# Kernel optimization log

Hardware: AMD Instinct MI355X
Metric: run time of the kernel (lower is better)

Reference implementation:

```python
import jax, jax.numpy as jnp
import numpy as np

B, S, D, H, OPS = 1024, 512, 128, 128, 16
V2 = 64000  # vocabulary_size * 2


def _lstm_last(emb, lengths, W_ih, W_hh, b_ih, b_hh, h0, c0):
    # emb: [B, S, D]; returns hidden state at step lengths-1 for each sample: [B, H]
    bsz = emb.shape[0]
    x = jnp.swapaxes(emb, 0, 1)  # [S, B, D]
    h = jnp.broadcast_to(h0[0], (bsz, h0.shape[-1]))  # learnable init state, expanded over batch
    c = jnp.broadcast_to(c0[0], (bsz, c0.shape[-1]))

    def step(carry, x_t):
        h, c = carry
        gates = x_t @ W_ih.T + b_ih + h @ W_hh.T + b_hh  # [B, 4H]
        i, f, g, o = jnp.split(gates, 4, axis=-1)  # torch LSTM gate order: i, f, g, o
        i = jax.nn.sigmoid(i); f = jax.nn.sigmoid(f)
        g = jnp.tanh(g); o = jax.nn.sigmoid(o)
        c = f * c + i * g
        h = o * jnp.tanh(c)
        return (h, c), h

    _, hs = jax.lax.scan(step, (h, c), x)  # hs: [S, B, H]
    t = jnp.maximum(lengths, 1) - 1  # last valid step per ragged sequence
    return hs[t, jnp.arange(bsz)]  # [B, H]


def setup_inputs() -> dict:
    key = jax.random.key(0)
    ks = jax.random.split(key, 12)
    sc = 0.05
    return {
        "tokens": jax.random.randint(ks[0], (B, S), 0, V2, dtype=jnp.int32),
        "lengths": jax.random.randint(ks[1], (B,), 1, S + 1, dtype=jnp.int32),
        "operator_onehot": jax.random.uniform(ks[2], (B, OPS), dtype=jnp.float32),
        "embedding": jax.random.normal(ks[3], (V2, D), dtype=jnp.float32) * sc,
        "W_ih": jax.random.normal(ks[4], (4 * H, D), dtype=jnp.float32) * sc,
        "W_hh": jax.random.normal(ks[5], (4 * H, H), dtype=jnp.float32) * sc,
        "b_ih": jax.random.normal(ks[6], (4 * H,), dtype=jnp.float32) * sc,
        "b_hh": jax.random.normal(ks[7], (4 * H,), dtype=jnp.float32) * sc,
        "h0": jnp.zeros((1, 1, H), dtype=jnp.float32),
        "c0": jnp.zeros((1, 1, H), dtype=jnp.float32),
        "lin_W": jax.random.normal(ks[8], (2, H + OPS), dtype=jnp.float32) * sc,
        "lin_b": jax.random.normal(ks[9], (2,), dtype=jnp.float32) * sc,
    }


def reference(tokens, lengths, operator_onehot, embedding, W_ih, W_hh, b_ih, b_hh, h0, c0, lin_W, lin_b):
    emb = jax.nn.relu(embedding[tokens])  # [B, S, D] embedding lookup + ReLU
    h_last = jax.nn.relu(_lstm_last(emb, lengths, W_ih, W_hh, b_ih, b_hh, h0, c0))  # [B, H]
    combined = jnp.concatenate([h_last, operator_onehot], axis=1)  # feature union
    return combined @ lin_W.T + lin_b  # [B, 2] logits (training mode: no sigmoid)
```

## Files before the change

kernel.cpp:

```cpp
#include <hip/hip_runtime.h>
#include <hip/hip_bf16.h>

#define NB    1024
#define SEQ   512
#define DIM   128
#define HID   128
#define NOPS  16
#define FEAT  144
#define BQ    4
#define AST   144
#define XST   578

typedef __bf16 bf16x8 __attribute__((ext_vector_type(8)));
typedef float  floatx4 __attribute__((ext_vector_type(4)));

__device__ __forceinline__ float gate_s(float aL, float aH, float ka) {
    const float kS = -1.4426950408889634f;
    const float arg = __builtin_fmaf(kS, aL, __builtin_fmaf(kS, aH, ka));
    return __builtin_amdgcn_rcpf(1.0f + __builtin_amdgcn_exp2f(arg));
}
__device__ __forceinline__ float gate_t(float aL, float aH, float ka) {
    const float kT = -2.8853900817779268f;
    const float arg = __builtin_fmaf(kT, aL, __builtin_fmaf(kT, aH, ka));
    return 2.0f * __builtin_amdgcn_rcpf(1.0f + __builtin_amdgcn_exp2f(arg)) - 1.0f;
}
__device__ __forceinline__ float tanh_c(float x) {
    const float kT = -2.8853900817779268f;
    return 2.0f * __builtin_amdgcn_rcpf(1.0f + __builtin_amdgcn_exp2f(kT * x)) - 1.0f;
}

__device__ __forceinline__ void block_sync_lds() {
    asm volatile("s_waitcnt lgkmcnt(0)\n\ts_barrier" ::: "memory");
}

__global__ __launch_bounds__(512, 2)
void lstm_fused(const int* __restrict__ tokens, const int* __restrict__ lengths,
                const float* __restrict__ onehot, const float* __restrict__ emb,
                const float* __restrict__ Wih, const float* __restrict__ Whh,
                const float* __restrict__ bih, const float* __restrict__ bhh,
                const float* __restrict__ h0, const float* __restrict__ c0,
                const float* __restrict__ linW, const float* __restrict__ linb,
                float* __restrict__ out)
{
    __shared__ __align__(16) __bf16 xbuf[8 * XST];
    __shared__ __align__(16) __bf16 hbuf[2 * BQ * AST];
    __shared__ __align__(16) float  hlbuf[BQ * HID];
    __shared__ __align__(16) int    tkbuf[BQ * SEQ];

    const int tid  = threadIdx.x;
    const int wave = tid >> 6;
    const int lane = tid & 63;
    const int quad = lane >> 4;
    const int lrow = lane & 15;
    const int bid  = blockIdx.x;

    bf16x8 wfx[4][4], wfh[4][4];
#pragma unroll
    for (int gt = 0; gt < 4; ++gt) {
        const int g = gt * 128 + wave * 16 + lrow;
#pragma unroll
        for (int kt = 0; kt < 4; ++kt) {
            const float* sx = Wih + g * DIM + kt * 32 + quad * 8;
            const float* sh = Whh + g * HID + kt * 32 + quad * 8;
            float4 a = *(const float4*)(sx);
            float4 b = *(const float4*)(sx + 4);
            bf16x8 v;
            v[0] = (__bf16)a.x; v[1] = (__bf16)a.y; v[2] = (__bf16)a.z; v[3] = (__bf16)a.w;
            v[4] = (__bf16)b.x; v[5] = (__bf16)b.y; v[6] = (__bf16)b.z; v[7] = (__bf16)b.w;
            wfx[gt][kt] = v;
            a = *(const float4*)(sh);
            b = *(const float4*)(sh + 4);
            v[0] = (__bf16)a.x; v[1] = (__bf16)a.y; v[2] = (__bf16)a.z; v[3] = (__bf16)a.w;
            v[4] = (__bf16)b.x; v[5] = (__bf16)b.y; v[6] = (__bf16)b.z; v[7] = (__bf16)b.w;
            wfh[gt][kt] = v;
        }
    }

    const int uu = wave * 16 + lrow;
    const int bq = bid * BQ + quad;
    int lenq = lengths[bq]; if (lenq < 1) lenq = 1;
    const int tlast = lenq - 1;

    int Lmax = 0;
#pragma unroll
    for (int s2 = 0; s2 < BQ; ++s2) {
        int l2 = lengths[bid * BQ + s2]; if (l2 < 1) l2 = 1;
        Lmax = (l2 > Lmax) ? l2 : Lmax;
    }

    const float kS = -1.4426950408889634f;
    const float kT = -2.8853900817779268f;
    const float karg0 = kS * (bih[0 * 128 + uu] + bhh[0 * 128 + uu]);
    const float karg1 = kS * (bih[1 * 128 + uu] + bhh[1 * 128 + uu]);
    const float karg2 = kT * (bih[2 * 128 + uu] + bhh[2 * 128 + uu]);
    const float karg3 = kS * (bih[3 * 128 + uu] + bhh[3 * 128 + uu]);

    float c  = c0[uu];
    float hl = 0.0f;

    const int m  = tid >> 7;
    const int u  = tid & 127;
    const int bm = bid * BQ + m;
    const int sm = m * AST + u;

    {
        const int4 tv = *(const int4*)(tokens + (size_t)bid * (BQ * SEQ) + tid * 4);
        *(int4*)(&tkbuf[tid * 4]) = tv;
    }

    hbuf[sm] = (__bf16)h0[u];
    const int* tokm = tokens + (size_t)bm * SEQ;
#pragma unroll
    for (int k = 0; k < 8; ++k) {
        float ek = emb[(size_t)tokm[k] * DIM + u];
        xbuf[k * XST + sm] = (__bf16)fmaxf(ek, 0.0f);
    }
    float e0 = emb[(size_t)tokm[8]  * DIM + u];
    float e1 = emb[(size_t)tokm[9]  * DIM + u];
    float e2 = emb[(size_t)tokm[10] * DIM + u];
    float e3 = emb[(size_t)tokm[11] * DIM + u];
    int   tk = tokm[12];

#define EREG(OFF) ((OFF) == 0 ? e0 : (OFF) == 1 ? e1 : (OFF) == 2 ? e2 : e3)

    const int xfbase = (lrow & 3) * XST + (lrow >> 2) * AST + quad * 8;
    const __bf16* const xfp[2] = { &xbuf[xfbase], &xbuf[4 * XST + xfbase] };
    const int habase = (lrow >> 2) * AST + quad * 8;
    const __bf16* const hf[2] = { &hbuf[habase], &hbuf[BQ * AST + habase] };
    __bf16* const hw[2] = { &hbuf[quad * AST + uu], &hbuf[BQ * AST + quad * AST + uu] };
    __bf16* const xw = &xbuf[sm];

    __syncthreads();

    const floatx4 zc = {0.0f, 0.0f, 0.0f, 0.0f};

    floatx4 xga[4], xgb[4];
#define XBLOCK(GRP, XGN) do {                                                        \
        bf16x8 af_[4];                                                               \
        _Pragma("unroll") for (int kt = 0; kt < 4; ++kt)                             \
            af_[kt] = *(const bf16x8*)(xfp[GRP] + kt * 32);                          \
        _Pragma("unroll") for (int gt = 0; gt < 4; ++gt)                             \
            XGN[gt] = __builtin_amdgcn_mfma_f32_16x16x32_bf16(af_[0], wfx[gt][0], zc, 0, 0, 0); \
        _Pragma("unroll") for (int kt = 1; kt < 4; ++kt)                             \
            _Pragma("unroll") for (int gt = 0; gt < 4; ++gt)                         \
                XGN[gt] = __builtin_amdgcn_mfma_f32_16x16x32_bf16(af_[kt], wfx[gt][kt], XGN[gt], 0, 0, 0); \
    } while (0)

    XBLOCK(0, xga);
    block_sync_lds();

#define STEP(G, OFF, XGC, XGN) do {                                                  \
        const int t  = ts + OFF;                                                     \
        bf16x8 ah_[4];                                                               \
        _Pragma("unroll") for (int kt = 0; kt < 4; ++kt)                             \
            ah_[kt] = *(const bf16x8*)(hf[OFF & 1] + kt * 32);                       \
        if (t + 8 < SEQ)         \
            xw[(4 * (G) + (OFF)) * XST] = (__bf16)fmaxf(EREG(OFF), 0.0f);            \
        if (t + 12 < SEQ)                                    \
            EREG(OFF) = emb[(size_t)tk * DIM + u];                                   \
        tk = tkbuf[m * SEQ + (((t + 13) < SEQ) ? (t + 13) : (SEQ - 1))];             \
        floatx4 aL[4], aH[4];                                                        \
        _Pragma("unroll") for (int gt = 0; gt < 4; ++gt)                             \
            aL[gt] = __builtin_amdgcn_mfma_f32_16x16x32_bf16(ah_[0], wfh[gt][0], XGC[gt], 0, 0, 0); \
        _Pragma("unroll") for (int gt = 0; gt < 4; ++gt)                             \
            aH[gt] = __builtin_amdgcn_mfma_f32_16x16x32_bf16(ah_[2], wfh[gt][2], zc, 0, 0, 0); \
        _Pragma("unroll") for (int gt = 0; gt < 4; ++gt)                             \
            aL[gt] = __builtin_amdgcn_mfma_f32_16x16x32_bf16(ah_[1], wfh[gt][1], aL[gt], 0, 0, 0); \
        _Pragma("unroll") for (int gt = 0; gt < 4; ++gt)                             \
            aH[gt] = __builtin_amdgcn_mfma_f32_16x16x32_bf16(ah_[3], wfh[gt][3], aH[gt], 0, 0, 0); \
        if (OFF == 0) { XBLOCK(1 - (G), XGN); }                                      \
        const float ii = gate_s(aL[0][OFF], aH[0][OFF], karg0);                      \
        const float ff = gate_s(aL[1][OFF], aH[1][OFF], karg1);                      \
        const float g2 = gate_t(aL[2][OFF], aH[2][OFF], karg2);                      \
        const float oo = gate_s(aL[3][OFF], aH[3][OFF], karg3);                      \
        c = ff * c + ii * g2;                                                        \
        const float h = oo * tanh_c(c);                                              \
        if (t == tlast) hl = fmaxf(h, 0.0f);                                         \
        *hw[1 - (OFF & 1)] = (__bf16)h;                                              \
        block_sync_lds();                                                            \
    } while (0)

    for (int ts8 = 0; ts8 < Lmax; ts8 += 8) {
        {
            const int ts = ts8;
            STEP(0, 0, xga, xgb); STEP(0, 1, xga, xgb);
            STEP(0, 2, xga, xgb); STEP(0, 3, xga, xgb);
        }
        {
            const int ts = ts8 + 4;
            STEP(1, 0, xgb, xga); STEP(1, 1, xgb, xga);
            STEP(1, 2, xgb, xga); STEP(1, 3, xgb, xga);
        }
    }
#undef STEP
#undef XBLOCK
#undef EREG

    hlbuf[quad * HID + uu] = hl;
    __syncthreads();
    if (tid < 2 * BQ) {
        const int mm = tid >> 1, kk = tid & 1;
        const int bb = bid * BQ + mm;
        float a2 = linb[kk];
        for (int q = 0; q < HID; ++q)
            a2 += hlbuf[mm * HID + q] * linW[kk * FEAT + q];
        for (int o = 0; o < NOPS; ++o)
            a2 += onehot[bb * NOPS + o] * linW[kk * FEAT + HID + o];
        out[bb * 2 + kk] = a2;
    }
}

extern "C" void kernel_launch(void* const* d_in, const int* in_sizes, int n_in,
                              void* d_out, int out_size, void* d_ws, size_t ws_size,
                              hipStream_t stream) {
    const int*   tokens  = (const int*)d_in[0];
    const int*   lengths = (const int*)d_in[1];
    const float* onehot  = (const float*)d_in[2];
    const float* emb     = (const float*)d_in[3];
    const float* Wih     = (const float*)d_in[4];
    const float* Whh     = (const float*)d_in[5];
    const float* bih     = (const float*)d_in[6];
    const float* bhh     = (const float*)d_in[7];
    const float* h0      = (const float*)d_in[8];
    const float* c0      = (const float*)d_in[9];
    const float* linW    = (const float*)d_in[10];
    const float* linb    = (const float*)d_in[11];
    float* out = (float*)d_out;
    (void)in_sizes; (void)n_in; (void)out_size; (void)d_ws; (void)ws_size;

    lstm_fused<<<dim3(NB / BQ), dim3(512), 0, stream>>>(
        tokens, lengths, onehot, emb, Wih, Whh, bih, bhh, h0, c0, linW, linb, out);
}
```

Measured before the change: 435.3 us.

## Spread next-group input projection MFMAs across the four recurrent steps

The input-projection block for the next group of four timesteps, previously issued all at once (16 MFMAs) in the first step, is now split so each step issues four MFMAs for one K slice. This balances MFMA work across steps on the serial recurrence critical path. The token buffer is also padded with zeros per row so the clamped index computation for the lookahead token fetch can be dropped. Correctness relies on each K slice of the x buffer being final before its step reads it, which the existing per-step barriers should ensure.

```diff
diff --git a/kernel.cpp b/kernel.cpp
--- a/kernel.cpp
+++ b/kernel.cpp
@@ -10,6 +10,7 @@
 #define BQ    4
 #define AST   144
 #define XST   578
+#define TKST  (SEQ + 16)
 
 typedef __bf16 bf16x8 __attribute__((ext_vector_type(8)));
 typedef float  floatx4 __attribute__((ext_vector_type(4)));
@@ -45,7 +46,7 @@
     __shared__ __align__(16) __bf16 xbuf[8 * XST];
     __shared__ __align__(16) __bf16 hbuf[2 * BQ * AST];
     __shared__ __align__(16) float  hlbuf[BQ * HID];
-    __shared__ __align__(16) int    tkbuf[BQ * SEQ];
+    __shared__ __align__(16) int    tkbuf[BQ * TKST];
 
     const int tid  = threadIdx.x;
     const int wave = tid >> 6;
@@ -104,8 +105,10 @@
     const int sm = m * AST + u;
 
     {
-        const int4 tv = *(const int4*)(tokens + (size_t)bid * (BQ * SEQ) + tid * 4);
-        *(int4*)(&tkbuf[tid * 4]) = tv;
+        const int4 tv = *(const int4*)(tokens + (size_t)bm * SEQ + (tid & 127) * 4);
+        *(int4*)(&tkbuf[m * TKST + (tid & 127) * 4]) = tv;
+        if (tid < BQ * 16)
+            tkbuf[(tid >> 4) * TKST + SEQ + (tid & 15)] = 0;
     }
 
     hbuf[sm] = (__bf16)h0[u];
@@ -135,40 +138,50 @@
     const floatx4 zc = {0.0f, 0.0f, 0.0f, 0.0f};
 
     floatx4 xga[4], xgb[4];
-#define XBLOCK(GRP, XGN) do {                                                        \
-        bf16x8 af_[4];                                                               \
-        _Pragma("unroll") for (int kt = 0; kt < 4; ++kt)                             \
-            af_[kt] = *(const bf16x8*)(xfp[GRP] + kt * 32);                          \
-        _Pragma("unroll") for (int gt = 0; gt < 4; ++gt)                             \
-            XGN[gt] = __builtin_amdgcn_mfma_f32_16x16x32_bf16(af_[0], wfx[gt][0], zc, 0, 0, 0); \
-        _Pragma("unroll") for (int kt = 1; kt < 4; ++kt)                             \
-            _Pragma("unroll") for (int gt = 0; gt < 4; ++gt)                         \
-                XGN[gt] = __builtin_amdgcn_mfma_f32_16x16x32_bf16(af_[kt], wfx[gt][kt], XGN[gt], 0, 0, 0); \
-    } while (0)
-
-    XBLOCK(0, xga);
+    {
+        bf16x8 af_[4];
+#pragma unroll
+        for (int kt = 0; kt < 4; ++kt)
+            af_[kt] = *(const bf16x8*)(xfp[0] + kt * 32);
+#pragma unroll
+        for (int gt = 0; gt < 4; ++gt)
+            xga[gt] = __builtin_amdgcn_mfma_f32_16x16x32_bf16(af_[0], wfx[gt][0], zc, 0, 0, 0);
+#pragma unroll
+        for (int kt = 1; kt < 4; ++kt)
+#pragma unroll
+            for (int gt = 0; gt < 4; ++gt)
+                xga[gt] = __builtin_amdgcn_mfma_f32_16x16x32_bf16(af_[kt], wfx[gt][kt], xga[gt], 0, 0, 0);
+    }
     block_sync_lds();
 
 #define STEP(G, OFF, XGC, XGN) do {                                                  \
         const int t  = ts + OFF;                                                     \
-        bf16x8 ah_[4];                                                               \
-        _Pragma("unroll") for (int kt = 0; kt < 4; ++kt)                             \
-            ah_[kt] = *(const bf16x8*)(hf[OFF & 1] + kt * 32);                       \
+        bf16x8 ah0 = *(const bf16x8*)(hf[OFF & 1] + 0 * 32);                         \
+        bf16x8 ah2 = *(const bf16x8*)(hf[OFF & 1] + 2 * 32);                         \
+        bf16x8 ah1 = *(const bf16x8*)(hf[OFF & 1] + 1 * 32);                         \
+        bf16x8 ah3 = *(const bf16x8*)(hf[OFF & 1] + 3 * 32);                         \
+        bf16x8 ax_ = *(const bf16x8*)(xfp[1 - (G)] + (OFF) * 32);                    \
         if (t + 8 < SEQ)         \
             xw[(4 * (G) + (OFF)) * XST] = (__bf16)fmaxf(EREG(OFF), 0.0f);            \
         if (t + 12 < SEQ)                                    \
             EREG(OFF) = emb[(size_t)tk * DIM + u];                                   \
-        tk = tkbuf[m * SEQ + (((t + 13) < SEQ) ? (t + 13) : (SEQ - 1))];             \
+        tk = tkbuf[m * TKST + t + 13];                                               \
         floatx4 aL[4], aH[4];                                                        \
         _Pragma("unroll") for (int gt = 0; gt < 4; ++gt)                             \
-            aL[gt] = __builtin_amdgcn_mfma_f32_16x16x32_bf16(ah_[0], wfh[gt][0], XGC[gt], 0, 0, 0); \
-        _Pragma("unroll") for (int gt = 0; gt < 4; ++gt)                             \
-            aH[gt] = __builtin_amdgcn_mfma_f32_16x16x32_bf16(ah_[2], wfh[gt][2], zc, 0, 0, 0); \
-        _Pragma("unroll") for (int gt = 0; gt < 4; ++gt)                             \
-            aL[gt] = __builtin_amdgcn_mfma_f32_16x16x32_bf16(ah_[1], wfh[gt][1], aL[gt], 0, 0, 0); \
-        _Pragma("unroll") for (int gt = 0; gt < 4; ++gt)                             \
-            aH[gt] = __builtin_amdgcn_mfma_f32_16x16x32_bf16(ah_[3], wfh[gt][3], aH[gt], 0, 0, 0); \
-        if (OFF == 0) { XBLOCK(1 - (G), XGN); }                                      \
+            aL[gt] = __builtin_amdgcn_mfma_f32_16x16x32_bf16(ah0, wfh[gt][0], XGC[gt], 0, 0, 0); \
+        _Pragma("unroll") for (int gt = 0; gt < 4; ++gt)                             \
+            aH[gt] = __builtin_amdgcn_mfma_f32_16x16x32_bf16(ah2, wfh[gt][2], zc, 0, 0, 0); \
+        _Pragma("unroll") for (int gt = 0; gt < 4; ++gt)                             \
+            aL[gt] = __builtin_amdgcn_mfma_f32_16x16x32_bf16(ah1, wfh[gt][1], aL[gt], 0, 0, 0); \
+        _Pragma("unroll") for (int gt = 0; gt < 4; ++gt)                             \
+            aH[gt] = __builtin_amdgcn_mfma_f32_16x16x32_bf16(ah3, wfh[gt][3], aH[gt], 0, 0, 0); \
+        if (OFF == 0) {                                                              \
+            _Pragma("unroll") for (int gt = 0; gt < 4; ++gt)                         \
+                XGN[gt] = __builtin_amdgcn_mfma_f32_16x16x32_bf16(ax_, wfx[gt][0], zc, 0, 0, 0); \
+        } else {                                                                     \
+            _Pragma("unroll") for (int gt = 0; gt < 4; ++gt)                         \
+                XGN[gt] = __builtin_amdgcn_mfma_f32_16x16x32_bf16(ax_, wfx[gt][OFF], XGN[gt], 0, 0, 0); \
+        }                                                                            \
         const float ii = gate_s(aL[0][OFF], aH[0][OFF], karg0);                      \
         const float ff = gate_s(aL[1][OFF], aH[1][OFF], karg1);                      \
         const float g2 = gate_t(aL[2][OFF], aH[2][OFF], karg2);                      \
@@ -193,7 +206,6 @@
         }
     }
 #undef STEP
-#undef XBLOCK
 #undef EREG
 
     hlbuf[quad * HID + uu] = hl;
```

Measured after the change: 421.8 us. 3.1% less time.
